# Kernel optimization log

Measured on AMD Instinct MI355X. Metric: run time of the kernel, lower is better.

## Reference

```python
import jax, jax.numpy as jnp
import numpy as np

N1 = 50000; N2 = 50000; E1 = 800000; E2 = 800000; A = 10000
D_IN = 128; NHID = 128; D_OUT = 128; RATIO = 0.5
N_SUP = int(N1 * RATIO)  # 25000 super nodes
K_HOPS = 10  # GCN(in, nhid, k=10)
NEG_INF = jnp.float32(-1e30)


def _edge_norm(src, dst, w, n):
    # symmetric degree normalization of edge weights
    deg = jax.ops.segment_sum(w, dst, num_segments=n) + 1.0
    return w * jax.lax.rsqrt(deg[src] * deg[dst])


def _prop(h, src, dst, norm, n):
    # one round of weighted message passing: h'[v] = sum_e norm_e * h[src_e]
    return jax.ops.segment_sum(norm[:, None] * h[src], dst, num_segments=n)


def _gcn_k(x, src, dst, norm, n, W, b):
    h = x @ W + b
    for _ in range(K_HOPS):
        h = _prop(h, src, dst, norm, n)
    return h


def setup_inputs() -> dict:
    key = jax.random.key(0)
    ks = jax.random.split(key, 24)
    s = 0.05
    return {
        "x": jax.random.normal(ks[0], (N1, D_IN), jnp.float32),
        "edge_index": jax.random.randint(ks[1], (2, E1), 0, N1, jnp.int32),
        "edge_weight": jax.random.uniform(ks[2], (E1,), jnp.float32),
        "y": jax.random.normal(ks[3], (N2, D_IN), jnp.float32),
        "edge_index_y": jax.random.randint(ks[4], (2, E2), 0, N2, jnp.int32),
        "edge_weight_y": jax.random.uniform(ks[5], (E2,), jnp.float32),
        "anchor_links": jax.random.randint(ks[6], (2, A), 0, N1, jnp.int32),
        "temperature": 1,
        "W_gcn": jax.random.normal(ks[7], (D_IN, NHID), jnp.float32) * s,
        "b_gcn": jnp.zeros((NHID,), jnp.float32),
        "p_score": jax.random.normal(ks[8], (NHID,), jnp.float32) * s,
        "W_conv1": jax.random.normal(ks[9], (NHID, NHID), jnp.float32) * s,
        "b_conv1": jnp.zeros((NHID,), jnp.float32),
        "W_mlp1": jax.random.normal(ks[10], (NHID, NHID), jnp.float32) * s,
        "b_mlp1": jnp.zeros((NHID,), jnp.float32),
        "W_l1": jax.random.normal(ks[11], (NHID, NHID), jnp.float32) * s,
        "W_l2": jax.random.normal(ks[12], (NHID, NHID), jnp.float32) * s,
        "W_mlp2": jax.random.normal(ks[13], (NHID, D_OUT), jnp.float32) * s,
        "b_mlp2": jnp.zeros((D_OUT,), jnp.float32),
    }


def reference(x, edge_index, edge_weight, y, edge_index_y, edge_weight_y,
              anchor_links, temperature, W_gcn, b_gcn, p_score, W_conv1,
              b_conv1, W_mlp1, b_mlp1, W_l1, W_l2, W_mlp2, b_mlp2):
    T = jnp.float32(temperature)
    src, dst = edge_index[0], edge_index[1]
    norm1 = _edge_norm(src, dst, edge_weight, N1)

    # ---- down_convs[0]: 10-hop GCN on graph 1 ----
    out_x = _gcn_k(x, src, dst, norm1, N1, W_gcn, b_gcn)  # xs[0]
    xr = jax.nn.relu(out_x)

    # ---- TransPool: score -> top-k super nodes -> attention assignment ----
    s = xr @ p_score                             # [N1]
    _, perm = jax.lax.top_k(s, N_SUP)            # original ids of super nodes
    sup_id = jnp.full((N1,), -1, jnp.int32).at[perm].set(
        jnp.arange(N_SUP, dtype=jnp.int32))
    self_ids = jnp.arange(N1, dtype=src.dtype)
    cand_node = jnp.concatenate([src, self_ids])  # node being assigned
    cand_sup = jnp.concatenate([dst, self_ids])   # candidate super node
    valid = sup_id[cand_sup] >= 0
    att = jnp.sum(xr[cand_node] * xr[cand_sup], axis=-1)
    att = att / (jnp.sqrt(jnp.float32(NHID)) * T)
    att = jnp.where(valid, att, NEG_INF)
    m = jax.ops.segment_max(att, cand_node, num_segments=N1)
    e = jnp.exp(att - m[cand_node])
    esum = jax.ops.segment_sum(e, cand_node, num_segments=N1)
    w_soft = e / esum[cand_node]                 # per-node softmax over candidates
    is_best = valid & (att >= m[cand_node])
    cluster = jnp.full((N1,), -1, jnp.int32).at[cand_node].max(
        jnp.where(is_best, sup_id[cand_sup], -1))
    has = cluster >= 0
    cluster = jnp.maximum(cluster, 0)
    match = is_best & (sup_id[cand_sup] == cluster[cand_node])
    a = jnp.zeros((N1,), jnp.float32).at[cand_node].max(
        jnp.where(match, w_soft, 0.0))
    a = jnp.where(has, a, 0.0)                   # assign_weight (P1 values)

    # coarsen: x' = P x ; A' = P A P^T via cluster relabeling
    x_pool = jax.ops.segment_sum(a[:, None] * xr, cluster, num_segments=N_SUP)
    csrc, cdst = cluster[src], cluster[dst]
    cw = edge_weight * a[src] * a[dst]

    # ---- down_convs[1]: GCNConv on coarse graph (with self loop) ----
    norm_c = _edge_norm(csrc, cdst, cw, N_SUP)
    h2 = x_pool @ W_conv1 + b_conv1
    h2 = _prop(h2, csrc, cdst, norm_c, N_SUP) + h2
    sup1 = jax.nn.relu(h2)                       # xs[1]

    # ---- MLP1 ----
    sup2 = jax.nn.relu(sup1 @ W_mlp1 + b_mlp1)

    # ---- Q = P1 @ L (sparse-sparse matmul) ----
    a1, a2 = anchor_links[0], anchor_links[1]
    anchor_w = jnp.ones((A,), jnp.float32)
    q_sup = cluster[a1]
    q_col = a2
    q_w = a[a1] * anchor_w

    # ---- graph 2: shared down_convs[0] ----
    srcy, dsty = edge_index_y[0], edge_index_y[1]
    normy = _edge_norm(srcy, dsty, edge_weight_y, N2)
    out_y = _gcn_k(y, srcy, dsty, normy, N2, W_gcn, b_gcn)

    # ---- LastLayer: Q^T (sup2 W_l1) + L^T (out_x W_l2) scattered into graph2 ----
    t1 = sup2 @ W_l1
    out_y = out_y + jax.ops.segment_sum(q_w[:, None] * t1[q_sup], q_col,
                                        num_segments=N2)
    t2 = out_x @ W_l2
    out_y = out_y + jax.ops.segment_sum(anchor_w[:, None] * t2[a1], a2,
                                        num_segments=N2)

    recon_y = out_y @ W_mlp2 + b_mlp2
    return (out_x, sup1, out_y, sup2, a, recon_y)
```

## Files before the change

### kernel.cpp

```cpp
#include <hip/hip_runtime.h>
#include <hip/hip_bf16.h>
#include <math.h>

#define N1 50000
#define N2 50000
#define E1C 800000
#define E2C 800000
#define AC 10000
#define F 128
#define NSUP 25000
#define KHOPS 10
#define NEGINF -1e30f
#define NBINS 65536
#define NBINS22 (1 << 22)

static inline int cdiv(int a, int b) { return (a + b - 1) / b; }

__device__ __forceinline__ float bf2f(unsigned short u) {
  return __uint_as_float(((unsigned)u) << 16);
}
__device__ __forceinline__ unsigned short f2bf(float f) {
  unsigned x = __float_as_uint(f);
  return (unsigned short)((x + 0x7FFFu + ((x >> 16) & 1u)) >> 16);
}

__global__ void k_deg_scatter(const int* __restrict__ dst, const float* __restrict__ w,
                              float* __restrict__ deg, int n) {
  int e = blockIdx.x * blockDim.x + threadIdx.x;
  if (e < n) atomicAdd(&deg[dst[e]], w[e]);
}

__global__ void k_edge_norm(const int* __restrict__ src, const int* __restrict__ dst,
                            const float* __restrict__ w, const float* __restrict__ deg,
                            float* __restrict__ norm, int n) {
  int e = blockIdx.x * blockDim.x + threadIdx.x;
  if (e < n) {
    float ds = deg[src[e]] + 1.0f, dd = deg[dst[e]] + 1.0f;
    norm[e] = w[e] / sqrtf(ds * dd);
  }
}

__global__ void k_count(const int* __restrict__ key, int* __restrict__ cnt, int n) {
  int e = blockIdx.x * blockDim.x + threadIdx.x;
  if (e < n) atomicAdd(&cnt[key[e]], 1);
}

__global__ void k_scan(const int* __restrict__ cnt, int* __restrict__ rowptr, int n) {
  const int T = 1024;
  int t = threadIdx.x;
  int vpt = (n + T - 1) / T;
  int lo = t * vpt, hi = lo + vpt;
  if (hi > n) hi = n;
  int sum = 0;
  for (int i = lo; i < hi; ++i) sum += cnt[i];
  int lane = t & 63, wid = t >> 6;
  int v = sum;
#pragma unroll
  for (int o = 1; o < 64; o <<= 1) {
    int u = __shfl_up(v, o, 64);
    if (lane >= o) v += u;
  }
  __shared__ int wsum[16];
  if (lane == 63) wsum[wid] = v;
  __syncthreads();
  if (t < 16) {
    int w = wsum[t];
#pragma unroll
    for (int o = 1; o < 16; o <<= 1) {
      int u = __shfl_up(w, o, 64);
      if (t >= o) w += u;
    }
    wsum[t] = w;
  }
  __syncthreads();
  int base = (wid ? wsum[wid - 1] : 0) + (v - sum);
  if (t == 0) rowptr[0] = 0;
  int run = base;
  for (int i = lo; i < hi; ++i) { run += cnt[i]; rowptr[i + 1] = run; }
}

__global__ void k_fill(const int* __restrict__ key, const int* __restrict__ payload,
                       const float* __restrict__ val, const int* __restrict__ rowptr,
                       int* __restrict__ cnt, int* __restrict__ col, float* __restrict__ v,
                       int n) {
  int e = blockIdx.x * blockDim.x + threadIdx.x;
  if (e < n) {
    int k = key[e];
    int p = atomicAdd(&cnt[k], 1);
    int s = rowptr[k] + p;
    col[s] = payload[e];
    if (val) v[s] = val[e];
  }
}

__global__ void k_count_coarse(const int* __restrict__ dst, const int* __restrict__ cluster,
                               int* __restrict__ cnt, int n) {
  int e = blockIdx.x * blockDim.x + threadIdx.x;
  if (e < n) atomicAdd(&cnt[cluster[dst[e]]], 1);
}

__global__ void k_fill_coarse(const int* __restrict__ src, const int* __restrict__ dst,
                              const int* __restrict__ cluster, const float* __restrict__ normc,
                              const int* __restrict__ rowptr, int* __restrict__ cnt,
                              int* __restrict__ col, float* __restrict__ v, int n) {
  int e = blockIdx.x * blockDim.x + threadIdx.x;
  if (e < n) {
    int k = cluster[dst[e]];
    int p = atomicAdd(&cnt[k], 1);
    int s = rowptr[k] + p;
    col[s] = cluster[src[e]];
    v[s] = normc[e];
  }
}

__global__ void k_prop(const float4* __restrict__ hin, float4* __restrict__ hout,
                       const int* __restrict__ rowptr, const int* __restrict__ col,
                       const float* __restrict__ val, int n) {
  int node = blockIdx.x * 8 + (threadIdx.x >> 5);
  if (node >= n) return;
  int q = threadIdx.x & 31;
  int s0 = rowptr[node], s1 = rowptr[node + 1];
  float4 acc = make_float4(0.f, 0.f, 0.f, 0.f);
  for (int s = s0; s < s1; s += 8) {
    int c[8]; float v[8];
#pragma unroll
    for (int j = 0; j < 8; ++j) {
      int ss = s + j;
      int sc = (ss < s1) ? ss : (s1 - 1);
      c[j] = col[sc];
      v[j] = (ss < s1) ? val[sc] : 0.f;
    }
    float4 h[8];
#pragma unroll
    for (int j = 0; j < 8; ++j) h[j] = hin[(size_t)c[j] * 32 + q];
#pragma unroll
    for (int j = 0; j < 8; ++j) {
      acc.x = fmaf(v[j], h[j].x, acc.x);
      acc.y = fmaf(v[j], h[j].y, acc.y);
      acc.z = fmaf(v[j], h[j].z, acc.z);
      acc.w = fmaf(v[j], h[j].w, acc.w);
    }
  }
  hout[(size_t)node * 32 + q] = acc;
}

__global__ void k_prop_bf16(const ushort4* __restrict__ hin, ushort4* __restrict__ hout,
                            float4* __restrict__ fout, const int* __restrict__ rowptr,
                            const int* __restrict__ col, const float* __restrict__ val, int n) {
  int node = blockIdx.x * 8 + (threadIdx.x >> 5);
  if (node >= n) return;
  int q = threadIdx.x & 31;
  int s0 = rowptr[node], s1 = rowptr[node + 1];
  float4 acc = make_float4(0.f, 0.f, 0.f, 0.f);
  for (int s = s0; s < s1; s += 8) {
    int c[8]; float v[8];
#pragma unroll
    for (int j = 0; j < 8; ++j) {
      int ss = s + j;
      int sc = (ss < s1) ? ss : (s1 - 1);
      c[j] = col[sc];
      v[j] = (ss < s1) ? val[sc] : 0.f;
    }
    ushort4 h[8];
#pragma unroll
    for (int j = 0; j < 8; ++j) h[j] = hin[(size_t)c[j] * 32 + q];
#pragma unroll
    for (int j = 0; j < 8; ++j) {
      acc.x = fmaf(v[j], bf2f(h[j].x), acc.x);
      acc.y = fmaf(v[j], bf2f(h[j].y), acc.y);
      acc.z = fmaf(v[j], bf2f(h[j].z), acc.z);
      acc.w = fmaf(v[j], bf2f(h[j].w), acc.w);
    }
  }
  if (fout) {
    fout[(size_t)node * 32 + q] = acc;
  } else {
    ushort4 o;
    o.x = f2bf(acc.x); o.y = f2bf(acc.y); o.z = f2bf(acc.z); o.w = f2bf(acc.w);
    hout[(size_t)node * 32 + q] = o;
  }
}

__global__ void k_transpose(const float* __restrict__ W, float* __restrict__ WT) {
  int i = blockIdx.x * blockDim.x + threadIdx.x;
  if (i < F * F) { int k = i >> 7, c = i & 127; WT[c * F + k] = W[i]; }
}

__global__ void k_mm128(const float* __restrict__ X, const float* __restrict__ WT,
                        const float* __restrict__ bias, float* __restrict__ out,
                        int M, int relu) {
  __shared__ float4 xs[16][32];
  int tid = threadIdx.x;
  int c = tid & 127;
  int half = tid >> 7;
  int row0 = blockIdx.x * 16;
  for (int t = tid; t < 512; t += 256) {
    int r = t >> 5, k4 = t & 31;
    int gr = row0 + r;
    float4 v = make_float4(0.f, 0.f, 0.f, 0.f);
    if (gr < M) v = ((const float4*)X)[(size_t)gr * 32 + k4];
    xs[r][k4] = v;
  }
  __syncthreads();
  float acc[8];
#pragma unroll
  for (int r = 0; r < 8; ++r) acc[r] = 0.f;
  const float4* wrow = (const float4*)WT + (size_t)c * 32;
  for (int k4 = 0; k4 < 32; ++k4) {
    float4 w = wrow[k4];
#pragma unroll
    for (int r = 0; r < 8; ++r) {
      float4 xv = xs[half * 8 + r][k4];
      acc[r] = fmaf(xv.x, w.x, acc[r]);
      acc[r] = fmaf(xv.y, w.y, acc[r]);
      acc[r] = fmaf(xv.z, w.z, acc[r]);
      acc[r] = fmaf(xv.w, w.w, acc[r]);
    }
  }
  float bb = bias ? bias[c] : 0.f;
#pragma unroll
  for (int r = 0; r < 8; ++r) {
    int gr = row0 + half * 8 + r;
    if (gr < M) {
      float v = acc[r] + bb;
      if (relu) v = fmaxf(v, 0.f);
      out[(size_t)gr * F + c] = v;
    }
  }
}

__global__ void k_mm128_bf16(const float* __restrict__ X, const float* __restrict__ WT,
                             const float* __restrict__ bias, unsigned short* __restrict__ out,
                             int M) {
  __shared__ float4 xs[16][32];
  int tid = threadIdx.x;
  int c = tid & 127;
  int half = tid >> 7;
  int row0 = blockIdx.x * 16;
  for (int t = tid; t < 512; t += 256) {
    int r = t >> 5, k4 = t & 31;
    int gr = row0 + r;
    float4 v = make_float4(0.f, 0.f, 0.f, 0.f);
    if (gr < M) v = ((const float4*)X)[(size_t)gr * 32 + k4];
    xs[r][k4] = v;
  }
  __syncthreads();
  float acc[8];
#pragma unroll
  for (int r = 0; r < 8; ++r) acc[r] = 0.f;
  const float4* wrow = (const float4*)WT + (size_t)c * 32;
  for (int k4 = 0; k4 < 32; ++k4) {
    float4 w = wrow[k4];
#pragma unroll
    for (int r = 0; r < 8; ++r) {
      float4 xv = xs[half * 8 + r][k4];
      acc[r] = fmaf(xv.x, w.x, acc[r]);
      acc[r] = fmaf(xv.y, w.y, acc[r]);
      acc[r] = fmaf(xv.z, w.z, acc[r]);
      acc[r] = fmaf(xv.w, w.w, acc[r]);
    }
  }
  float bb = bias ? bias[c] : 0.f;
#pragma unroll
  for (int r = 0; r < 8; ++r) {
    int gr = row0 + half * 8 + r;
    if (gr < M) out[(size_t)gr * F + c] = f2bf(acc[r] + bb);
  }
}

__global__ void k_relu4(const float4* __restrict__ in, float4* __restrict__ out, int n4) {
  int i = blockIdx.x * blockDim.x + threadIdx.x;
  if (i < n4) {
    float4 v = in[i];
    v.x = fmaxf(v.x, 0.f); v.y = fmaxf(v.y, 0.f);
    v.z = fmaxf(v.z, 0.f); v.w = fmaxf(v.w, 0.f);
    out[i] = v;
  }
}

__global__ void k_addrelu(const float* __restrict__ a, const float* __restrict__ b,
                          float* __restrict__ out, int n) {
  int i = blockIdx.x * blockDim.x + threadIdx.x;
  if (i < n) out[i] = fmaxf(a[i] + b[i], 0.f);
}

__global__ void k_score(const float* __restrict__ xr, const float* __restrict__ p,
                        float* __restrict__ s, int n) {
  int wid = (blockIdx.x * blockDim.x + threadIdx.x) >> 6;
  int lane = threadIdx.x & 63;
  if (wid >= n) return;
  const float* row = xr + (size_t)wid * F;
  float d = row[lane] * p[lane] + row[lane + 64] * p[lane + 64];
#pragma unroll
  for (int o = 32; o; o >>= 1) d += __shfl_xor(d, o, 64);
  if (lane == 0) s[wid] = d;
}

__device__ __forceinline__ unsigned sortkey(float f) {
  if (f == 0.f) f = 0.f;
  unsigned u = __float_as_uint(f);
  return (u & 0x80000000u) ? ~u : (u | 0x80000000u);
}

__global__ void k_key(const float* __restrict__ s, unsigned* __restrict__ key, int n) {
  int i = blockIdx.x * blockDim.x + threadIdx.x;
  if (i < n) key[i] = sortkey(s[i]);
}

__global__ void k_count_bins22(const unsigned* __restrict__ key, int* __restrict__ cnt, int n) {
  int i = blockIdx.x * blockDim.x + threadIdx.x;
  if (i < n) atomicAdd(&cnt[key[i] >> 10], 1);
}

__global__ void k_hist_blocksum(const int* __restrict__ cnt, int* __restrict__ partial) {
  int t = threadIdx.x;
  int base = blockIdx.x * 1024 + t * 4;
  int s = cnt[base] + cnt[base + 1] + cnt[base + 2] + cnt[base + 3];
#pragma unroll
  for (int o = 32; o; o >>= 1) s += __shfl_down(s, o, 64);
  __shared__ int ws[4];
  int lane = t & 63, w = t >> 6;
  if (lane == 0) ws[w] = s;
  __syncthreads();
  if (t == 0) partial[blockIdx.x] = ws[0] + ws[1] + ws[2] + ws[3];
}

__global__ void k_hist_apply(const int* __restrict__ cnt, const int* __restrict__ partialptr,
                             int* __restrict__ binptr) {
  int t = threadIdx.x;
  int base = blockIdx.x * 1024 + t * 4;
  int c0 = cnt[base], c1 = cnt[base + 1], c2 = cnt[base + 2], c3 = cnt[base + 3];
  int s = c0 + c1 + c2 + c3;
  int lane = t & 63, w = t >> 6;
  int v = s;
#pragma unroll
  for (int o = 1; o < 64; o <<= 1) {
    int u = __shfl_up(v, o, 64);
    if (lane >= o) v += u;
  }
  __shared__ int ws[4];
  if (lane == 63) ws[w] = v;
  __syncthreads();
  int wb = 0;
  for (int i = 0; i < w; ++i) wb += ws[i];
  int run = partialptr[blockIdx.x] + wb + (v - s);
  binptr[base + 1] = run + c0;
  binptr[base + 2] = run + c0 + c1;
  binptr[base + 3] = run + c0 + c1 + c2;
  binptr[base + 4] = run + s;
  if (blockIdx.x == 0 && t == 0) binptr[0] = 0;
}

__global__ void k_fill_bins22(const unsigned* __restrict__ key, const int* __restrict__ binptr,
                              int* __restrict__ cnt, int* __restrict__ bidx,
                              unsigned* __restrict__ bkey, int n) {
  int i = blockIdx.x * blockDim.x + threadIdx.x;
  if (i < n) {
    unsigned k = key[i];
    int b = k >> 10;
    int p = atomicAdd(&cnt[b], 1);
    int s = binptr[b] + p;
    bidx[s] = i;
    bkey[s] = k;
  }
}

__global__ void k_rank22(const unsigned* __restrict__ key, const int* __restrict__ binptr,
                         const int* __restrict__ bidx, const unsigned* __restrict__ bkey,
                         int* __restrict__ supid, int n) {
  int i = blockIdx.x * blockDim.x + threadIdx.x;
  if (i >= n) return;
  unsigned ki = key[i];
  int b = ki >> 10;
  int cnt = n - binptr[b + 1];
  int s1 = binptr[b + 1];
  for (int s = binptr[b]; s < s1; ++s) {
    unsigned kj = bkey[s];
    cnt += (kj > ki) || (kj == ki && bidx[s] < i);
  }
  supid[i] = (cnt < NSUP) ? cnt : -1;
}

__device__ __forceinline__ float read_T(const void* p) {
  int ib = *(const int*)p;
  float fb = __int_as_float(ib);
  if (ib >= 1 && ib < (1 << 20)) return (float)ib;
  if (fb > 1e-6f && fb < 1e6f) return fb;
  return 1.0f;
}

__global__ void k_att_a(const float* __restrict__ xr, const int* __restrict__ rowptr,
                        const int* __restrict__ col, const int* __restrict__ supid,
                        const void* __restrict__ tptr, float* __restrict__ att,
                        float* __restrict__ attself, float* __restrict__ mout, int n) {
  int wid = (blockIdx.x * blockDim.x + threadIdx.x) >> 6;
  int lane = threadIdx.x & 63;
  if (wid >= n) return;
  float inv = 1.0f / (sqrtf(128.0f) * read_T(tptr));
  const float* xn = xr + (size_t)wid * F;
  float x0 = xn[lane], x1 = xn[lane + 64];
  float d = x0 * x0 + x1 * x1;
#pragma unroll
  for (int o = 32; o; o >>= 1) d += __shfl_xor(d, o, 64);
  float av = (supid[wid] >= 0) ? d * inv : NEGINF;
  float m = av;
  if (lane == 0) attself[wid] = av;
  int s0 = rowptr[wid], s1 = rowptr[wid + 1];
  for (int s = s0; s < s1; s += 4) {
    int c[4]; bool ok[4];
#pragma unroll
    for (int j = 0; j < 4; ++j) {
      int ss = s + j;
      ok[j] = ss < s1;
      c[j] = col[ok[j] ? ss : (s1 - 1)];
    }
    float dd[4];
#pragma unroll
    for (int j = 0; j < 4; ++j) {
      const float* xc = xr + (size_t)c[j] * F;
      dd[j] = x0 * xc[lane] + x1 * xc[lane + 64];
    }
#pragma unroll
    for (int j = 0; j < 4; ++j) {
#pragma unroll
      for (int o = 32; o; o >>= 1) dd[j] += __shfl_xor(dd[j], o, 64);
    }
#pragma unroll
    for (int j = 0; j < 4; ++j) {
      if (ok[j]) {
        float a2 = (supid[c[j]] >= 0) ? dd[j] * inv : NEGINF;
        if (lane == 0) att[s + j] = a2;
        m = fmaxf(m, a2);
      }
    }
  }
  if (lane == 0) mout[wid] = m;
}

__global__ void k_att_b(const int* __restrict__ rowptr, const int* __restrict__ col,
                        const int* __restrict__ supid, const float* __restrict__ att,
                        const float* __restrict__ attself, const float* __restrict__ mv,
                        int* __restrict__ cluster, float* __restrict__ aout, int n) {
  int i = blockIdx.x * blockDim.x + threadIdx.x;
  if (i >= n) return;
  float m = mv[i];
  float as = attself[i];
  float esum = expf(as - m);
  int best = -1;
  if (as >= m) {
    int sid = supid[i];
    if (sid > best) best = sid;
  }
  int s0 = rowptr[i], s1 = rowptr[i + 1];
  for (int s = s0; s < s1; ++s) {
    float av = att[s];
    esum += expf(av - m);
    if (av >= m) {
      int sid = supid[col[s]];
      if (sid > best) best = sid;
    }
  }
  int has = best >= 0;
  cluster[i] = has ? best : 0;
  aout[i] = has ? 1.0f / esum : 0.0f;
}

__global__ void k_xpool(const float* __restrict__ xr, const float* __restrict__ a,
                        const int* __restrict__ cluster, float* __restrict__ xpool, int total) {
  int idx = blockIdx.x * blockDim.x + threadIdx.x;
  if (idx >= total) return;
  int node = idx >> 7;
  float av = a[node];
  if (av != 0.f) atomicAdd(&xpool[(size_t)cluster[node] * F + (idx & 127)], av * xr[idx]);
}

__global__ void k_cdeg(const int* __restrict__ src, const int* __restrict__ dst,
                       const float* __restrict__ w, const float* __restrict__ a,
                       const int* __restrict__ cluster, float* __restrict__ degc, int n) {
  int e = blockIdx.x * blockDim.x + threadIdx.x;
  if (e < n) {
    float cw = w[e] * a[src[e]] * a[dst[e]];
    if (cw != 0.f) atomicAdd(&degc[cluster[dst[e]]], cw);
  }
}

__global__ void k_cnorm(const int* __restrict__ src, const int* __restrict__ dst,
                        const float* __restrict__ w, const float* __restrict__ a,
                        const int* __restrict__ cluster, const float* __restrict__ degc,
                        float* __restrict__ normc, int n) {
  int e = blockIdx.x * blockDim.x + threadIdx.x;
  if (e < n) {
    float cw = w[e] * a[src[e]] * a[dst[e]];
    float ds = degc[cluster[src[e]]] + 1.f, dd = degc[cluster[dst[e]]] + 1.f;
    normc[e] = cw / sqrtf(ds * dd);
  }
}

__global__ void k_scatter_q(const int* __restrict__ a1, const int* __restrict__ a2,
                            const int* __restrict__ cluster, const float* __restrict__ aarr,
                            const float* __restrict__ t1, float* __restrict__ outy, int nA) {
  int idx = blockIdx.x * blockDim.x + threadIdx.x;
  if (idx >= nA * F) return;
  int k = idx >> 7, f = idx & 127;
  int n1 = a1[k];
  float qw = aarr[n1];
  if (qw != 0.f)
    atomicAdd(&outy[(size_t)a2[k] * F + f], qw * t1[(size_t)cluster[n1] * F + f]);
}

__global__ void k_scatter_t2(const int* __restrict__ a1, const int* __restrict__ a2,
                             const float* __restrict__ t2, float* __restrict__ outy, int nA) {
  int idx = blockIdx.x * blockDim.x + threadIdx.x;
  if (idx >= nA * F) return;
  int k = idx >> 7, f = idx & 127;
  atomicAdd(&outy[(size_t)a2[k] * F + f], t2[(size_t)a1[k] * F + f]);
}

extern "C" void kernel_launch(void* const* d_in, const int* in_sizes, int n_in,
                              void* d_out, int out_size, void* d_ws, size_t ws_size,
                              hipStream_t stream) {
  (void)in_sizes; (void)n_in; (void)out_size; (void)ws_size;
  const float* x   = (const float*)d_in[0];
  const int*   ei  = (const int*)d_in[1];
  const float* w1  = (const float*)d_in[2];
  const float* y   = (const float*)d_in[3];
  const int*   eiy = (const int*)d_in[4];
  const float* wy  = (const float*)d_in[5];
  const int*   anc = (const int*)d_in[6];
  const void*  tmp = d_in[7];
  const float* W_gcn = (const float*)d_in[8];
  const float* b_gcn = (const float*)d_in[9];
  const float* p_sc  = (const float*)d_in[10];
  const float* W_c1  = (const float*)d_in[11];
  const float* b_c1  = (const float*)d_in[12];
  const float* W_m1  = (const float*)d_in[13];
  const float* b_m1  = (const float*)d_in[14];
  const float* W_l1  = (const float*)d_in[15];
  const float* W_l2  = (const float*)d_in[16];
  const float* W_m2  = (const float*)d_in[17];
  const float* b_m2  = (const float*)d_in[18];

  float* out   = (float*)d_out;
  float* out_x = out;
  float* sup1  = out_x + (size_t)N1 * F;
  float* out_y = sup1 + (size_t)NSUP * F;
  float* sup2  = out_y + (size_t)N2 * F;
  float* a_out = sup2 + (size_t)NSUP * F;
  float* recon = a_out + N1;

  char* wsb = (char*)d_ws;
  size_t off = 0;
  auto alloc = [&](size_t bytes) -> void* {
    void* p = wsb + off;
    off = (off + bytes + 255) & ~(size_t)255;
    return p;
  };
  float*    f_norm1   = (float*)alloc((size_t)E1C * 4);
  float*    f_csr1v   = (float*)alloc((size_t)E1C * 4);
  int*      i_csr1c   = (int*)alloc((size_t)E1C * 4);
  int*      i_rowptr1 = (int*)alloc((size_t)(N1 + 1) * 4);
  float*    f_deg     = (float*)alloc((size_t)N1 * 4);
  int*      i_cnt     = (int*)alloc((size_t)(NBINS + 1) * 4);
  float*    f_ha      = (float*)alloc((size_t)N1 * F * 4);
  float*    f_hb      = (float*)alloc((size_t)N1 * F * 4);
  float*    f_xr      = (float*)alloc((size_t)N1 * F * 4);
  float*    f_s       = (float*)alloc((size_t)N1 * 4);
  unsigned* u_key     = (unsigned*)alloc((size_t)N1 * 4);
  int*      i_partial = (int*)alloc((size_t)4096 * 4);
  int*      i_partptr = (int*)alloc((size_t)4097 * 4);
  int*      i_bidx    = (int*)alloc((size_t)N1 * 4);
  unsigned* u_bkey    = (unsigned*)alloc((size_t)N1 * 4);
  int*      i_supid   = (int*)alloc((size_t)N1 * 4);
  int*      i_rowptrS = (int*)alloc((size_t)(N1 + 1) * 4);
  int*      i_csrSc   = (int*)alloc((size_t)E1C * 4);
  float*    f_att     = (float*)alloc((size_t)E1C * 4);
  float*    f_attself = (float*)alloc((size_t)N1 * 4);
  float*    f_m       = (float*)alloc((size_t)N1 * 4);
  int*      i_cluster = (int*)alloc((size_t)N1 * 4);
  float*    f_xpool   = (float*)alloc((size_t)NSUP * F * 4);
  float*    f_degc    = (float*)alloc((size_t)NSUP * 4);
  float*    f_normc   = (float*)alloc((size_t)E1C * 4);
  int*      i_rowptrC = (int*)alloc((size_t)(NSUP + 1) * 4);
  int*      i_csrCc   = (int*)alloc((size_t)E1C * 4);
  float*    f_csrCv   = (float*)alloc((size_t)E1C * 4);
  float*    f_h2      = (float*)alloc((size_t)NSUP * F * 4);
  float*    f_h2p     = (float*)alloc((size_t)NSUP * F * 4);
  float*    f_wt      = (float*)alloc((size_t)6 * F * F * 4);

  int* i_cnt22    = (int*)f_ha;
  int* i_binptr22 = (int*)f_hb;
  unsigned short* h16a = (unsigned short*)f_ha;
  unsigned short* h16b = (unsigned short*)f_hb;

  const int* src1 = ei,  * dst1 = ei + E1C;
  const int* srcy = eiy, * dsty = eiy + E2C;
  const int* a1 = anc, * a2 = anc + AC;

  const float* Ws[6] = { W_gcn, W_c1, W_m1, W_l1, W_l2, W_m2 };
  for (int i = 0; i < 6; ++i)
    k_transpose<<<cdiv(F * F, 256), 256, 0, stream>>>(Ws[i], f_wt + (size_t)i * F * F);
  float* wt_gcn = f_wt, *wt_c1 = f_wt + 16384, *wt_m1 = f_wt + 2 * 16384,
       * wt_l1 = f_wt + 3 * 16384, *wt_l2 = f_wt + 4 * 16384, *wt_m2 = f_wt + 5 * 16384;

  int gE = cdiv(E1C, 256);

  hipMemsetAsync(f_deg, 0, (size_t)N1 * 4, stream);
  k_deg_scatter<<<gE, 256, 0, stream>>>(dst1, w1, f_deg, E1C);
  k_edge_norm<<<gE, 256, 0, stream>>>(src1, dst1, w1, f_deg, f_norm1, E1C);

  hipMemsetAsync(i_cnt, 0, (size_t)(NBINS + 1) * 4, stream);
  k_count<<<gE, 256, 0, stream>>>(dst1, i_cnt, E1C);
  k_scan<<<1, 1024, 0, stream>>>(i_cnt, i_rowptr1, N1);
  hipMemsetAsync(i_cnt, 0, (size_t)(NBINS + 1) * 4, stream);
  k_fill<<<gE, 256, 0, stream>>>(dst1, src1, f_norm1, i_rowptr1, i_cnt, i_csr1c, f_csr1v, E1C);

  k_mm128<<<cdiv(N1, 16), 256, 0, stream>>>(x, wt_gcn, b_gcn, f_ha, N1, 0);
  {
    const float* cur = f_ha;
    for (int i = 0; i < KHOPS; ++i) {
      float* dst = (i == KHOPS - 1) ? out_x : ((i & 1) ? f_ha : f_hb);
      k_prop<<<cdiv(N1, 8), 256, 0, stream>>>((const float4*)cur, (float4*)dst,
                                              i_rowptr1, i_csr1c, f_csr1v, N1);
      cur = dst;
    }
  }
  k_relu4<<<cdiv(N1 * F / 4, 256), 256, 0, stream>>>((const float4*)out_x, (float4*)f_xr, N1 * F / 4);

  k_score<<<cdiv(N1, 4), 256, 0, stream>>>(f_xr, p_sc, f_s, N1);
  k_key<<<cdiv(N1, 256), 256, 0, stream>>>(f_s, u_key, N1);
  hipMemsetAsync(i_cnt22, 0, (size_t)NBINS22 * 4, stream);
  k_count_bins22<<<cdiv(N1, 256), 256, 0, stream>>>(u_key, i_cnt22, N1);
  k_hist_blocksum<<<NBINS22 / 1024, 256, 0, stream>>>(i_cnt22, i_partial);
  k_scan<<<1, 1024, 0, stream>>>(i_partial, i_partptr, 4096);
  k_hist_apply<<<NBINS22 / 1024, 256, 0, stream>>>(i_cnt22, i_partptr, i_binptr22);
  hipMemsetAsync(i_cnt22, 0, (size_t)NBINS22 * 4, stream);
  k_fill_bins22<<<cdiv(N1, 256), 256, 0, stream>>>(u_key, i_binptr22, i_cnt22, i_bidx, u_bkey, N1);
  k_rank22<<<cdiv(N1, 256), 256, 0, stream>>>(u_key, i_binptr22, i_bidx, u_bkey, i_supid, N1);

  hipMemsetAsync(i_cnt, 0, (size_t)(NBINS + 1) * 4, stream);
  k_count<<<gE, 256, 0, stream>>>(src1, i_cnt, E1C);
  k_scan<<<1, 1024, 0, stream>>>(i_cnt, i_rowptrS, N1);
  hipMemsetAsync(i_cnt, 0, (size_t)(NBINS + 1) * 4, stream);
  k_fill<<<gE, 256, 0, stream>>>(src1, dst1, (const float*)nullptr, i_rowptrS, i_cnt, i_csrSc,
                                 (float*)nullptr, E1C);

  k_att_a<<<cdiv(N1, 4), 256, 0, stream>>>(f_xr, i_rowptrS, i_csrSc, i_supid, tmp,
                                           f_att, f_attself, f_m, N1);
  k_att_b<<<cdiv(N1, 256), 256, 0, stream>>>(i_rowptrS, i_csrSc, i_supid, f_att, f_attself,
                                             f_m, i_cluster, a_out, N1);

  hipMemsetAsync(f_xpool, 0, (size_t)NSUP * F * 4, stream);
  k_xpool<<<cdiv(N1 * F, 256), 256, 0, stream>>>(f_xr, a_out, i_cluster, f_xpool, N1 * F);
  hipMemsetAsync(f_degc, 0, (size_t)NSUP * 4, stream);
  k_cdeg<<<gE, 256, 0, stream>>>(src1, dst1, w1, a_out, i_cluster, f_degc, E1C);
  k_cnorm<<<gE, 256, 0, stream>>>(src1, dst1, w1, a_out, i_cluster, f_degc, f_normc, E1C);
  hipMemsetAsync(i_cnt, 0, (size_t)(NBINS + 1) * 4, stream);
  k_count_coarse<<<gE, 256, 0, stream>>>(dst1, i_cluster, i_cnt, E1C);
  k_scan<<<1, 1024, 0, stream>>>(i_cnt, i_rowptrC, NSUP);
  hipMemsetAsync(i_cnt, 0, (size_t)(NBINS + 1) * 4, stream);
  k_fill_coarse<<<gE, 256, 0, stream>>>(src1, dst1, i_cluster, f_normc, i_rowptrC, i_cnt,
                                        i_csrCc, f_csrCv, E1C);

  k_mm128<<<cdiv(NSUP, 16), 256, 0, stream>>>(f_xpool, wt_c1, b_c1, f_h2, NSUP, 0);
  k_prop<<<cdiv(NSUP, 8), 256, 0, stream>>>((const float4*)f_h2, (float4*)f_h2p,
                                            i_rowptrC, i_csrCc, f_csrCv, NSUP);
  k_addrelu<<<cdiv(NSUP * F, 256), 256, 0, stream>>>(f_h2p, f_h2, sup1, NSUP * F);
  k_mm128<<<cdiv(NSUP, 16), 256, 0, stream>>>(sup1, wt_m1, b_m1, sup2, NSUP, 1);

  hipMemsetAsync(f_deg, 0, (size_t)N2 * 4, stream);
  k_deg_scatter<<<gE, 256, 0, stream>>>(dsty, wy, f_deg, E2C);
  k_edge_norm<<<gE, 256, 0, stream>>>(srcy, dsty, wy, f_deg, f_norm1, E2C);
  hipMemsetAsync(i_cnt, 0, (size_t)(NBINS + 1) * 4, stream);
  k_count<<<gE, 256, 0, stream>>>(dsty, i_cnt, E2C);
  k_scan<<<1, 1024, 0, stream>>>(i_cnt, i_rowptr1, N2);
  hipMemsetAsync(i_cnt, 0, (size_t)(NBINS + 1) * 4, stream);
  k_fill<<<gE, 256, 0, stream>>>(dsty, srcy, f_norm1, i_rowptr1, i_cnt, i_csr1c, f_csr1v, E2C);
  k_mm128_bf16<<<cdiv(N2, 16), 256, 0, stream>>>(y, wt_gcn, b_gcn, h16a, N2);
  {
    const unsigned short* cur = h16a;
    for (int i = 0; i < KHOPS; ++i) {
      int last = (i == KHOPS - 1);
      unsigned short* dst = (i & 1) ? h16a : h16b;
      k_prop_bf16<<<cdiv(N2, 8), 256, 0, stream>>>(
          (const ushort4*)cur, last ? nullptr : (ushort4*)dst,
          last ? (float4*)out_y : nullptr, i_rowptr1, i_csr1c, f_csr1v, N2);
      cur = dst;
    }
  }

  float* f_t1 = f_h2p;
  float* f_t2 = f_xr;
  k_mm128<<<cdiv(NSUP, 16), 256, 0, stream>>>(sup2, wt_l1, (const float*)nullptr, f_t1, NSUP, 0);
  k_scatter_q<<<cdiv(AC * F, 256), 256, 0, stream>>>(a1, a2, i_cluster, a_out, f_t1, out_y, AC);
  k_mm128<<<cdiv(N1, 16), 256, 0, stream>>>(out_x, wt_l2, (const float*)nullptr, f_t2, N1, 0);
  k_scatter_t2<<<cdiv(AC * F, 256), 256, 0, stream>>>(a1, a2, f_t2, out_y, AC);

  k_mm128<<<cdiv(N2, 16), 256, 0, stream>>>(out_y, wt_m2, b_m2, recon, N2, 0);
}
```

Measured before the change: 2.557 ms.

## Compute edge norms in CSR order, pull-based pooling, fuse final ReLU into prop

```diff
diff --git a/kernel.cpp b/kernel.cpp
--- a/kernel.cpp
+++ b/kernel.cpp
@@ -24,22 +24,6 @@
   return (unsigned short)((x + 0x7FFFu + ((x >> 16) & 1u)) >> 16);
 }
 
-__global__ void k_deg_scatter(const int* __restrict__ dst, const float* __restrict__ w,
-                              float* __restrict__ deg, int n) {
-  int e = blockIdx.x * blockDim.x + threadIdx.x;
-  if (e < n) atomicAdd(&deg[dst[e]], w[e]);
-}
-
-__global__ void k_edge_norm(const int* __restrict__ src, const int* __restrict__ dst,
-                            const float* __restrict__ w, const float* __restrict__ deg,
-                            float* __restrict__ norm, int n) {
-  int e = blockIdx.x * blockDim.x + threadIdx.x;
-  if (e < n) {
-    float ds = deg[src[e]] + 1.0f, dd = deg[dst[e]] + 1.0f;
-    norm[e] = w[e] / sqrtf(ds * dd);
-  }
-}
-
 __global__ void k_count(const int* __restrict__ key, int* __restrict__ cnt, int n) {
   int e = blockIdx.x * blockDim.x + threadIdx.x;
   if (e < n) atomicAdd(&cnt[key[e]], 1);
@@ -93,6 +77,16 @@
   }
 }
 
+__global__ void k_fill_iota(const int* __restrict__ key, const int* __restrict__ rowptr,
+                            int* __restrict__ cnt, int* __restrict__ col, int n) {
+  int e = blockIdx.x * blockDim.x + threadIdx.x;
+  if (e < n) {
+    int k = key[e];
+    int p = atomicAdd(&cnt[k], 1);
+    col[rowptr[k] + p] = e;
+  }
+}
+
 __global__ void k_count_coarse(const int* __restrict__ dst, const int* __restrict__ cluster,
                                int* __restrict__ cnt, int n) {
   int e = blockIdx.x * blockDim.x + threadIdx.x;
@@ -100,22 +94,58 @@
 }
 
 __global__ void k_fill_coarse(const int* __restrict__ src, const int* __restrict__ dst,
-                              const int* __restrict__ cluster, const float* __restrict__ normc,
-                              const int* __restrict__ rowptr, int* __restrict__ cnt,
-                              int* __restrict__ col, float* __restrict__ v, int n) {
+                              const int* __restrict__ cluster, const float* __restrict__ w,
+                              const float* __restrict__ a, const int* __restrict__ rowptr,
+                              int* __restrict__ cnt, int* __restrict__ col,
+                              float* __restrict__ v, int n) {
   int e = blockIdx.x * blockDim.x + threadIdx.x;
   if (e < n) {
-    int k = cluster[dst[e]];
+    int sd = dst[e];
+    int k = cluster[sd];
     int p = atomicAdd(&cnt[k], 1);
     int s = rowptr[k] + p;
-    col[s] = cluster[src[e]];
-    v[s] = normc[e];
+    int ss = src[e];
+    col[s] = cluster[ss];
+    v[s] = w[e] * a[ss] * a[sd];
+  }
+}
+
+__global__ void k_rowsum(const int* __restrict__ rowptr, const float* __restrict__ v,
+                         float* __restrict__ deg, int n) {
+  int i = blockIdx.x * blockDim.x + threadIdx.x;
+  if (i >= n) return;
+  int s0 = rowptr[i], s1 = rowptr[i + 1];
+  float s = 0.f;
+  for (int k = s0; k < s1; ++k) s += v[k];
+  deg[i] = s;
+}
+
+__global__ void k_csrnorm(const int* __restrict__ rowptr, const int* __restrict__ col,
+                          float* __restrict__ v, const float* __restrict__ deg, int n) {
+  int i = blockIdx.x * blockDim.x + threadIdx.x;
+  if (i >= n) return;
+  int s0 = rowptr[i], s1 = rowptr[i + 1];
+  float di = deg[i] + 1.f;
+  for (int s = s0; s < s1; s += 4) {
+    int c[4]; bool ok[4];
+#pragma unroll
+    for (int j = 0; j < 4; ++j) {
+      int ss = s + j;
+      ok[j] = ss < s1;
+      c[j] = col[ok[j] ? ss : (s1 - 1)];
+    }
+    float dc[4];
+#pragma unroll
+    for (int j = 0; j < 4; ++j) dc[j] = deg[c[j]];
+#pragma unroll
+    for (int j = 0; j < 4; ++j)
+      if (ok[j]) v[s + j] = v[s + j] / sqrtf((dc[j] + 1.f) * di);
   }
 }
 
 __global__ void k_prop(const float4* __restrict__ hin, float4* __restrict__ hout,
-                       const int* __restrict__ rowptr, const int* __restrict__ col,
-                       const float* __restrict__ val, int n) {
+                       float4* __restrict__ relu_out, const int* __restrict__ rowptr,
+                       const int* __restrict__ col, const float* __restrict__ val, int n) {
   int node = blockIdx.x * 8 + (threadIdx.x >> 5);
   if (node >= n) return;
   int q = threadIdx.x & 31;
@@ -142,6 +172,12 @@
     }
   }
   hout[(size_t)node * 32 + q] = acc;
+  if (relu_out) {
+    float4 r;
+    r.x = fmaxf(acc.x, 0.f); r.y = fmaxf(acc.y, 0.f);
+    r.z = fmaxf(acc.z, 0.f); r.w = fmaxf(acc.w, 0.f);
+    relu_out[(size_t)node * 32 + q] = r;
+  }
 }
 
 __global__ void k_prop_bf16(const ushort4* __restrict__ hin, ushort4* __restrict__ hout,
@@ -268,16 +304,6 @@
   }
 }
 
-__global__ void k_relu4(const float4* __restrict__ in, float4* __restrict__ out, int n4) {
-  int i = blockIdx.x * blockDim.x + threadIdx.x;
-  if (i < n4) {
-    float4 v = in[i];
-    v.x = fmaxf(v.x, 0.f); v.y = fmaxf(v.y, 0.f);
-    v.z = fmaxf(v.z, 0.f); v.w = fmaxf(v.w, 0.f);
-    out[i] = v;
-  }
-}
-
 __global__ void k_addrelu(const float* __restrict__ a, const float* __restrict__ b,
                           float* __restrict__ out, int n) {
   int i = blockIdx.x * blockDim.x + threadIdx.x;
@@ -465,35 +491,24 @@
   aout[i] = has ? 1.0f / esum : 0.0f;
 }
 
-__global__ void k_xpool(const float* __restrict__ xr, const float* __restrict__ a,
-                        const int* __restrict__ cluster, float* __restrict__ xpool, int total) {
-  int idx = blockIdx.x * blockDim.x + threadIdx.x;
-  if (idx >= total) return;
-  int node = idx >> 7;
-  float av = a[node];
-  if (av != 0.f) atomicAdd(&xpool[(size_t)cluster[node] * F + (idx & 127)], av * xr[idx]);
-}
-
-__global__ void k_cdeg(const int* __restrict__ src, const int* __restrict__ dst,
-                       const float* __restrict__ w, const float* __restrict__ a,
-                       const int* __restrict__ cluster, float* __restrict__ degc, int n) {
-  int e = blockIdx.x * blockDim.x + threadIdx.x;
-  if (e < n) {
-    float cw = w[e] * a[src[e]] * a[dst[e]];
-    if (cw != 0.f) atomicAdd(&degc[cluster[dst[e]]], cw);
-  }
-}
-
-__global__ void k_cnorm(const int* __restrict__ src, const int* __restrict__ dst,
-                        const float* __restrict__ w, const float* __restrict__ a,
-                        const int* __restrict__ cluster, const float* __restrict__ degc,
-                        float* __restrict__ normc, int n) {
-  int e = blockIdx.x * blockDim.x + threadIdx.x;
-  if (e < n) {
-    float cw = w[e] * a[src[e]] * a[dst[e]];
-    float ds = degc[cluster[src[e]]] + 1.f, dd = degc[cluster[dst[e]]] + 1.f;
-    normc[e] = cw / sqrtf(ds * dd);
-  }
+__global__ void k_xpool_pull(const float4* __restrict__ xr, const float* __restrict__ a,
+                             const int* __restrict__ rowptrM, const int* __restrict__ memb,
+                             float4* __restrict__ xpool, int n) {
+  int c = blockIdx.x * 8 + (threadIdx.x >> 5);
+  if (c >= n) return;
+  int q = threadIdx.x & 31;
+  int s0 = rowptrM[c], s1 = rowptrM[c + 1];
+  float4 acc = make_float4(0.f, 0.f, 0.f, 0.f);
+  for (int s = s0; s < s1; ++s) {
+    int m = memb[s];
+    float av = a[m];
+    float4 h = xr[(size_t)m * 32 + q];
+    acc.x = fmaf(av, h.x, acc.x);
+    acc.y = fmaf(av, h.y, acc.y);
+    acc.z = fmaf(av, h.z, acc.z);
+    acc.w = fmaf(av, h.w, acc.w);
+  }
+  xpool[(size_t)c * 32 + q] = acc;
 }
 
 __global__ void k_scatter_q(const int* __restrict__ a1, const int* __restrict__ a2,
@@ -555,7 +570,6 @@
     off = (off + bytes + 255) & ~(size_t)255;
     return p;
   };
-  float*    f_norm1   = (float*)alloc((size_t)E1C * 4);
   float*    f_csr1v   = (float*)alloc((size_t)E1C * 4);
   int*      i_csr1c   = (int*)alloc((size_t)E1C * 4);
   int*      i_rowptr1 = (int*)alloc((size_t)(N1 + 1) * 4);
@@ -579,10 +593,11 @@
   int*      i_cluster = (int*)alloc((size_t)N1 * 4);
   float*    f_xpool   = (float*)alloc((size_t)NSUP * F * 4);
   float*    f_degc    = (float*)alloc((size_t)NSUP * 4);
-  float*    f_normc   = (float*)alloc((size_t)E1C * 4);
   int*      i_rowptrC = (int*)alloc((size_t)(NSUP + 1) * 4);
   int*      i_csrCc   = (int*)alloc((size_t)E1C * 4);
   float*    f_csrCv   = (float*)alloc((size_t)E1C * 4);
+  int*      i_rowptrM = (int*)alloc((size_t)(NSUP + 1) * 4);
+  int*      i_memb    = (int*)alloc((size_t)N1 * 4);
   float*    f_h2      = (float*)alloc((size_t)NSUP * F * 4);
   float*    f_h2p     = (float*)alloc((size_t)NSUP * F * 4);
   float*    f_wt      = (float*)alloc((size_t)6 * F * F * 4);
@@ -603,39 +618,39 @@
        * wt_l1 = f_wt + 3 * 16384, *wt_l2 = f_wt + 4 * 16384, *wt_m2 = f_wt + 5 * 16384;
 
   int gE = cdiv(E1C, 256);
-
-  hipMemsetAsync(f_deg, 0, (size_t)N1 * 4, stream);
-  k_deg_scatter<<<gE, 256, 0, stream>>>(dst1, w1, f_deg, E1C);
-  k_edge_norm<<<gE, 256, 0, stream>>>(src1, dst1, w1, f_deg, f_norm1, E1C);
+  int gN = cdiv(N1, 256);
 
   hipMemsetAsync(i_cnt, 0, (size_t)(NBINS + 1) * 4, stream);
   k_count<<<gE, 256, 0, stream>>>(dst1, i_cnt, E1C);
   k_scan<<<1, 1024, 0, stream>>>(i_cnt, i_rowptr1, N1);
   hipMemsetAsync(i_cnt, 0, (size_t)(NBINS + 1) * 4, stream);
-  k_fill<<<gE, 256, 0, stream>>>(dst1, src1, f_norm1, i_rowptr1, i_cnt, i_csr1c, f_csr1v, E1C);
+  k_fill<<<gE, 256, 0, stream>>>(dst1, src1, w1, i_rowptr1, i_cnt, i_csr1c, f_csr1v, E1C);
+  k_rowsum<<<gN, 256, 0, stream>>>(i_rowptr1, f_csr1v, f_deg, N1);
+  k_csrnorm<<<gN, 256, 0, stream>>>(i_rowptr1, i_csr1c, f_csr1v, f_deg, N1);
 
   k_mm128<<<cdiv(N1, 16), 256, 0, stream>>>(x, wt_gcn, b_gcn, f_ha, N1, 0);
   {
     const float* cur = f_ha;
     for (int i = 0; i < KHOPS; ++i) {
-      float* dst = (i == KHOPS - 1) ? out_x : ((i & 1) ? f_ha : f_hb);
+      int last = (i == KHOPS - 1);
+      float* dst = last ? out_x : ((i & 1) ? f_ha : f_hb);
       k_prop<<<cdiv(N1, 8), 256, 0, stream>>>((const float4*)cur, (float4*)dst,
+                                              last ? (float4*)f_xr : nullptr,
                                               i_rowptr1, i_csr1c, f_csr1v, N1);
       cur = dst;
     }
   }
-  k_relu4<<<cdiv(N1 * F / 4, 256), 256, 0, stream>>>((const float4*)out_x, (float4*)f_xr, N1 * F / 4);
 
   k_score<<<cdiv(N1, 4), 256, 0, stream>>>(f_xr, p_sc, f_s, N1);
-  k_key<<<cdiv(N1, 256), 256, 0, stream>>>(f_s, u_key, N1);
+  k_key<<<gN, 256, 0, stream>>>(f_s, u_key, N1);
   hipMemsetAsync(i_cnt22, 0, (size_t)NBINS22 * 4, stream);
-  k_count_bins22<<<cdiv(N1, 256), 256, 0, stream>>>(u_key, i_cnt22, N1);
+  k_count_bins22<<<gN, 256, 0, stream>>>(u_key, i_cnt22, N1);
   k_hist_blocksum<<<NBINS22 / 1024, 256, 0, stream>>>(i_cnt22, i_partial);
   k_scan<<<1, 1024, 0, stream>>>(i_partial, i_partptr, 4096);
   k_hist_apply<<<NBINS22 / 1024, 256, 0, stream>>>(i_cnt22, i_partptr, i_binptr22);
   hipMemsetAsync(i_cnt22, 0, (size_t)NBINS22 * 4, stream);
-  k_fill_bins22<<<cdiv(N1, 256), 256, 0, stream>>>(u_key, i_binptr22, i_cnt22, i_bidx, u_bkey, N1);
-  k_rank22<<<cdiv(N1, 256), 256, 0, stream>>>(u_key, i_binptr22, i_bidx, u_bkey, i_supid, N1);
+  k_fill_bins22<<<gN, 256, 0, stream>>>(u_key, i_binptr22, i_cnt22, i_bidx, u_bkey, N1);
+  k_rank22<<<gN, 256, 0, stream>>>(u_key, i_binptr22, i_bidx, u_bkey, i_supid, N1);
 
   hipMemsetAsync(i_cnt, 0, (size_t)(NBINS + 1) * 4, stream);
   k_count<<<gE, 256, 0, stream>>>(src1, i_cnt, E1C);
@@ -646,35 +661,39 @@
 
   k_att_a<<<cdiv(N1, 4), 256, 0, stream>>>(f_xr, i_rowptrS, i_csrSc, i_supid, tmp,
                                            f_att, f_attself, f_m, N1);
-  k_att_b<<<cdiv(N1, 256), 256, 0, stream>>>(i_rowptrS, i_csrSc, i_supid, f_att, f_attself,
-                                             f_m, i_cluster, a_out, N1);
-
-  hipMemsetAsync(f_xpool, 0, (size_t)NSUP * F * 4, stream);
-  k_xpool<<<cdiv(N1 * F, 256), 256, 0, stream>>>(f_xr, a_out, i_cluster, f_xpool, N1 * F);
-  hipMemsetAsync(f_degc, 0, (size_t)NSUP * 4, stream);
-  k_cdeg<<<gE, 256, 0, stream>>>(src1, dst1, w1, a_out, i_cluster, f_degc, E1C);
-  k_cnorm<<<gE, 256, 0, stream>>>(src1, dst1, w1, a_out, i_cluster, f_degc, f_normc, E1C);
+  k_att_b<<<gN, 256, 0, stream>>>(i_rowptrS, i_csrSc, i_supid, f_att, f_attself,
+                                  f_m, i_cluster, a_out, N1);
+
+  hipMemsetAsync(i_cnt, 0, (size_t)(NBINS + 1) * 4, stream);
+  k_count<<<gN, 256, 0, stream>>>(i_cluster, i_cnt, N1);
+  k_scan<<<1, 1024, 0, stream>>>(i_cnt, i_rowptrM, NSUP);
+  hipMemsetAsync(i_cnt, 0, (size_t)(NBINS + 1) * 4, stream);
+  k_fill_iota<<<gN, 256, 0, stream>>>(i_cluster, i_rowptrM, i_cnt, i_memb, N1);
+  k_xpool_pull<<<cdiv(NSUP, 8), 256, 0, stream>>>((const float4*)f_xr, a_out, i_rowptrM,
+                                                  i_memb, (float4*)f_xpool, NSUP);
+
   hipMemsetAsync(i_cnt, 0, (size_t)(NBINS + 1) * 4, stream);
   k_count_coarse<<<gE, 256, 0, stream>>>(dst1, i_cluster, i_cnt, E1C);
   k_scan<<<1, 1024, 0, stream>>>(i_cnt, i_rowptrC, NSUP);
   hipMemsetAsync(i_cnt, 0, (size_t)(NBINS + 1) * 4, stream);
-  k_fill_coarse<<<gE, 256, 0, stream>>>(src1, dst1, i_cluster, f_normc, i_rowptrC, i_cnt,
+  k_fill_coarse<<<gE, 256, 0, stream>>>(src1, dst1, i_cluster, w1, a_out, i_rowptrC, i_cnt,
                                         i_csrCc, f_csrCv, E1C);
+  k_rowsum<<<cdiv(NSUP, 256), 256, 0, stream>>>(i_rowptrC, f_csrCv, f_degc, NSUP);
+  k_csrnorm<<<cdiv(NSUP, 256), 256, 0, stream>>>(i_rowptrC, i_csrCc, f_csrCv, f_degc, NSUP);
 
   k_mm128<<<cdiv(NSUP, 16), 256, 0, stream>>>(f_xpool, wt_c1, b_c1, f_h2, NSUP, 0);
-  k_prop<<<cdiv(NSUP, 8), 256, 0, stream>>>((const float4*)f_h2, (float4*)f_h2p,
+  k_prop<<<cdiv(NSUP, 8), 256, 0, stream>>>((const float4*)f_h2, (float4*)f_h2p, nullptr,
                                             i_rowptrC, i_csrCc, f_csrCv, NSUP);
   k_addrelu<<<cdiv(NSUP * F, 256), 256, 0, stream>>>(f_h2p, f_h2, sup1, NSUP * F);
   k_mm128<<<cdiv(NSUP, 16), 256, 0, stream>>>(sup1, wt_m1, b_m1, sup2, NSUP, 1);
 
-  hipMemsetAsync(f_deg, 0, (size_t)N2 * 4, stream);
-  k_deg_scatter<<<gE, 256, 0, stream>>>(dsty, wy, f_deg, E2C);
-  k_edge_norm<<<gE, 256, 0, stream>>>(srcy, dsty, wy, f_deg, f_norm1, E2C);
   hipMemsetAsync(i_cnt, 0, (size_t)(NBINS + 1) * 4, stream);
   k_count<<<gE, 256, 0, stream>>>(dsty, i_cnt, E2C);
   k_scan<<<1, 1024, 0, stream>>>(i_cnt, i_rowptr1, N2);
   hipMemsetAsync(i_cnt, 0, (size_t)(NBINS + 1) * 4, stream);
-  k_fill<<<gE, 256, 0, stream>>>(dsty, srcy, f_norm1, i_rowptr1, i_cnt, i_csr1c, f_csr1v, E2C);
+  k_fill<<<gE, 256, 0, stream>>>(dsty, srcy, wy, i_rowptr1, i_cnt, i_csr1c, f_csr1v, E2C);
+  k_rowsum<<<gN, 256, 0, stream>>>(i_rowptr1, f_csr1v, f_deg, N2);
+  k_csrnorm<<<gN, 256, 0, stream>>>(i_rowptr1, i_csr1c, f_csr1v, f_deg, N2);
   k_mm128_bf16<<<cdiv(N2, 16), 256, 0, stream>>>(y, wt_gcn, b_gcn, h16a, N2);
   {
     const unsigned short* cur = h16a;
```

Measured after the change: 2.667 ms. 4.3% more time.
